# Kernel tuning notes

Hardware: AMD Instinct MI355X
Metric: run time of the kernel (lower is better)

The kernel has to match this reference:

```python
import jax, jax.numpy as jnp
import numpy as np

B, L, H = 2, 2048, 1536
I, N, R, K = 3072, 16, 96, 4


def setup_inputs() -> dict:
    key = jax.random.key(0)
    ks = jax.random.split(key, 10)
    rn = lambda k, shape, s: jax.random.normal(k, shape, jnp.float32) * s
    return {
        "hidden_states": rn(ks[0], (B, L, H), 1.0),
        "W_in": rn(ks[1], (2 * I, H), 0.02),
        "conv_w": rn(ks[2], (I, K), 0.1),
        "conv_b": rn(ks[3], (I,), 0.1),
        "W_x": rn(ks[4], (R + 2 * N, I), 0.02),
        "W_dt": rn(ks[5], (I, R), 0.02),
        "dt_bias": rn(ks[6], (I,), 0.1),
        # vLLM's weight loader stores A = -exp(A_log); replicate that here
        "A": -jnp.exp(rn(ks[7], (I, N), 0.5)),
        "D": jnp.ones((I,), jnp.float32),
        "W_out": rn(ks[8], (H, I), 0.02),
    }


def reference(hidden_states, W_in, conv_w, conv_b, W_x, W_dt, dt_bias, A, D, W_out):
    b, l, _ = hidden_states.shape
    k = conv_w.shape[1]
    n = A.shape[1]
    r = W_dt.shape[1]

    # in_proj -> [B,L,2I], split into ssm input x and gate
    proj = jnp.einsum("blh,eh->ble", hidden_states, W_in)
    x, gate = jnp.split(proj, 2, axis=-1)  # each [B,L,I]

    # causal depthwise conv1d over L (pad K-1 on the left) + SiLU
    xp = jnp.pad(x, ((0, 0), (k - 1, 0), (0, 0)))
    conv = sum(xp[:, j : j + l, :] * conv_w[:, j] for j in range(k)) + conv_b
    x = jax.nn.silu(conv)  # [B,L,I]

    # x_proj -> dt (rank R), B, C (each N)
    ssm_p = jnp.einsum("bli,pi->blp", x, W_x)
    dt_in, Bm, Cm = jnp.split(ssm_p, [r, r + n], axis=-1)

    # dt_proj (skip_bias_add) then softplus(dt + bias) inside the scan math
    dt = jnp.einsum("blr,ir->bli", dt_in, W_dt)
    delta = jax.nn.softplus(dt + dt_bias)  # [B,L,I]

    # selective scan: s_t = exp(delta_t * A) * s_{t-1} + delta_t * x_t * B_t
    def step(state, inp):
        d_t, u_t, B_t, C_t = inp  # [B,I], [B,I], [B,N], [B,N]
        dA = jnp.exp(d_t[..., None] * A)  # [B,I,N]
        state = state * dA + (d_t * u_t)[..., None] * B_t[:, None, :]
        y = jnp.einsum("bin,bn->bi", state, C_t)
        return state, y

    init = jnp.zeros((b, x.shape[-1], n), jnp.float32)
    _, ys = jax.lax.scan(
        step,
        init,
        (
            delta.transpose(1, 0, 2),
            x.transpose(1, 0, 2),
            Bm.transpose(1, 0, 2),
            Cm.transpose(1, 0, 2),
        ),
    )
    y = ys.transpose(1, 0, 2) + x * D  # skip connection via D
    y = y * jax.nn.silu(gate)

    # out_proj -> [B,L,H]
    return jnp.einsum("bli,hi->blh", y, W_out)
```

## Files before the change

kernel.cpp:

```cpp
#include <hip/hip_runtime.h>

typedef __attribute__((ext_vector_type(8))) short bf16x8;
typedef __attribute__((ext_vector_type(4))) float f32x4;

#define CCH 32
#define TCH 64

__device__ __forceinline__ unsigned short f2b(float f) {
    unsigned u = __float_as_uint(f);
    return (unsigned short)((u + 0x7fffu + ((u >> 16) & 1u)) >> 16);
}
__device__ __forceinline__ float b2f(unsigned short h) {
    return __uint_as_float(((unsigned)h) << 16);
}
__device__ __forceinline__ float softplus_f(float z) {
    return (z > 15.f) ? z : __logf(1.f + __expf(z));
}
__device__ __forceinline__ float silu_f(float g) {
    return g / (1.f + __expf(-g));
}

__device__ __forceinline__ void gload16(const unsigned short* g, unsigned short* l) {
    __builtin_amdgcn_global_load_lds(
        (const __attribute__((address_space(1))) void*)g,
        (__attribute__((address_space(3))) void*)l, 16, 0, 0);
}

__global__ __launch_bounds__(256)
void cast_all(const float* __restrict__ h, const float* __restrict__ win,
              const float* __restrict__ wx, const float* __restrict__ wdt,
              const float* __restrict__ wout,
              unsigned short* __restrict__ dh, unsigned short* __restrict__ dwin,
              unsigned short* __restrict__ dwx, unsigned short* __restrict__ dwdt,
              unsigned short* __restrict__ dwout) {
    const int n0 = 1572864, n1 = n0 + 2359296, n2 = n1 + 98304,
              n3 = n2 + 73728, n4 = n3 + 1179648;
    int i = blockIdx.x * 256 + threadIdx.x;
    const float* s; unsigned short* d; int off;
    if (i < n0)      { s = h;    d = dh;    off = i; }
    else if (i < n1) { s = win;  d = dwin;  off = i - n0; }
    else if (i < n2) { s = wx;   d = dwx;   off = i - n1; }
    else if (i < n3) { s = wdt;  d = dwdt;  off = i - n2; }
    else if (i < n4) { s = wout; d = dwout; off = i - n3; }
    else return;
    float4 v = reinterpret_cast<const float4*>(s)[off];
    ushort4 o;
    o.x = f2b(v.x); o.y = f2b(v.y); o.z = f2b(v.z); o.w = f2b(v.w);
    reinterpret_cast<ushort4*>(d)[off] = o;
}

template <int OP>
__global__ __launch_bounds__(512)
void gemm256(const unsigned short* __restrict__ A, const unsigned short* __restrict__ W,
             void* __restrict__ Cout, int Kc, int lda, int ldw, int ldc,
             int ntx, int silu_col0, long long czs) {
    __shared__ __align__(16) unsigned short lds[65536];
    const int tid  = threadIdx.x;
    const int lane = tid & 63;
    const int wave = tid >> 6;
    const int wr   = wave >> 2;
    const int wc   = wave & 3;
    const int lr   = lane & 15;
    const int quad = lane >> 4;
    const int sw   = lr & 7;

    const int nwg = gridDim.x;
    const int wg  = blockIdx.x;
    const int wgs = (wg & 7) * (nwg >> 3) + (wg >> 3);
    const int bm  = (wgs / ntx) * 256;
    const int bn  = (wgs % ntx) * 256;
    const int kz  = blockIdx.z;
    A += (size_t)kz * Kc;
    W += (size_t)kz * Kc;

    const int rsub = wave * 8 + (lane >> 3);
    const int csw  = ((lane & 7) ^ ((lane >> 3) & 7)) * 8;
    const unsigned short* gA = A + (size_t)(bm + rsub) * lda + csw;
    const unsigned short* gB = W + (size_t)(bn + rsub) * ldw + csw;

#define STA(b, h, kt) do { \
        gload16(gA + (size_t)((h) * 128) * lda + (kt) * 64,      &lds[(b) * 16384 + (h) * 8192 + wave * 512]); \
        gload16(gA + (size_t)((h) * 128 + 64) * lda + (kt) * 64, &lds[(b) * 16384 + (h) * 8192 + 4096 + wave * 512]); \
    } while (0)
#define STB(b, h, kt) do { \
        gload16(gB + (size_t)((h) * 128) * ldw + (kt) * 64,      &lds[32768 + (b) * 16384 + (h) * 8192 + wave * 512]); \
        gload16(gB + (size_t)((h) * 128 + 64) * ldw + (kt) * 64, &lds[32768 + (b) * 16384 + (h) * 8192 + 4096 + wave * 512]); \
    } while (0)

#define LDA_F(b, mh, mi, kk) \
    (*reinterpret_cast<const bf16x8*>(&lds[(b) * 16384 + ((mh) * 128 + wr * 64 + (mi) * 16 + lr) * 64 + (((((kk) << 2) | quad)) ^ sw) * 8]))
#define LDB_F(b, nh, ni, kk) \
    (*reinterpret_cast<const bf16x8*>(&lds[32768 + (b) * 16384 + ((nh) * 128 + wc * 32 + (ni) * 16 + lr) * 64 + (((((kk) << 2) | quad)) ^ sw) * 8]))

#define RD_A(b, mh) do { \
        _Pragma("unroll") for (int mi = 0; mi < 4; ++mi) { \
            fa[mi][0] = LDA_F(b, mh, mi, 0); \
            fa[mi][1] = LDA_F(b, mh, mi, 1); } } while (0)
#define RD_B(b, nh, dst) do { \
        _Pragma("unroll") for (int ni = 0; ni < 2; ++ni) { \
            dst[ni][0] = LDB_F(b, nh, ni, 0); \
            dst[ni][1] = LDB_F(b, nh, ni, 1); } } while (0)

#define MFMA_Q(mh, nh, bb) do { \
        _Pragma("unroll") for (int mi = 0; mi < 4; ++mi) \
        _Pragma("unroll") for (int ni = 0; ni < 2; ++ni) { \
            acc[(mh) * 4 + mi][(nh) * 2 + ni] = __builtin_amdgcn_mfma_f32_16x16x32_bf16(fa[mi][0], bb[ni][0], acc[(mh) * 4 + mi][(nh) * 2 + ni], 0, 0, 0); \
            acc[(mh) * 4 + mi][(nh) * 2 + ni] = __builtin_amdgcn_mfma_f32_16x16x32_bf16(fa[mi][1], bb[ni][1], acc[(mh) * 4 + mi][(nh) * 2 + ni], 0, 0, 0); } } while (0)

#define MIDB  asm volatile("s_barrier" ::: "memory")
#define LGKM0 asm volatile("s_waitcnt lgkmcnt(0)" ::: "memory")
#define ENDB  asm volatile("s_barrier" ::: "memory")
#define ENDB_VM4 asm volatile("s_waitcnt vmcnt(4)\n\ts_barrier" ::: "memory")
#define ENDB_VM0 asm volatile("s_waitcnt vmcnt(0)\n\ts_barrier" ::: "memory")
#define PRIO1 __builtin_amdgcn_s_setprio(1)
#define PRIO0 __builtin_amdgcn_s_setprio(0)

    f32x4 acc[8][4];
    const f32x4 zero = {0.f, 0.f, 0.f, 0.f};
#pragma unroll
    for (int m = 0; m < 8; ++m)
#pragma unroll
        for (int n = 0; n < 4; ++n) acc[m][n] = zero;

    bf16x8 fa[4][2], fb0[2][2], fb1[2][2];

    const int nkt = Kc >> 6;
    const int NT2 = nkt >> 1;

    STA(0, 0, 0); STB(0, 0, 0); STA(0, 1, 0); STB(0, 1, 0);
    STA(1, 0, 1); STB(1, 0, 1);
    ENDB_VM4;

#pragma unroll 1
    for (int t = 0; t < NT2 - 1; ++t) {
        const int k1 = 2 * t + 1, k2 = 2 * t + 2, k3 = 2 * t + 3;
        RD_A(0, 0); RD_B(0, 0, fb0); STA(1, 1, k1);
        MIDB; LGKM0; PRIO1; MFMA_Q(0, 0, fb0); PRIO0; ENDB;
        RD_B(0, 1, fb1); STB(1, 1, k1);
        MIDB; LGKM0; PRIO1; MFMA_Q(0, 1, fb1); PRIO0; ENDB;
        RD_A(0, 1); STA(0, 0, k2);
        MIDB; LGKM0; PRIO1; MFMA_Q(1, 0, fb0); PRIO0; ENDB;
        STB(0, 0, k2);
        MIDB; PRIO1; MFMA_Q(1, 1, fb1); PRIO0; ENDB_VM4;
        RD_A(1, 0); RD_B(1, 0, fb0); STA(0, 1, k2);
        MIDB; LGKM0; PRIO1; MFMA_Q(0, 0, fb0); PRIO0; ENDB;
        RD_B(1, 1, fb1); STB(0, 1, k2);
        MIDB; LGKM0; PRIO1; MFMA_Q(0, 1, fb1); PRIO0; ENDB;
        RD_A(1, 1); STA(1, 0, k3);
        MIDB; LGKM0; PRIO1; MFMA_Q(1, 0, fb0); PRIO0; ENDB;
        STB(1, 0, k3);
        MIDB; PRIO1; MFMA_Q(1, 1, fb1); PRIO0; ENDB_VM4;
    }
    {
        const int k1 = nkt - 1;
        RD_A(0, 0); RD_B(0, 0, fb0); STA(1, 1, k1);
        MIDB; LGKM0; PRIO1; MFMA_Q(0, 0, fb0); PRIO0; ENDB;
        RD_B(0, 1, fb1); STB(1, 1, k1);
        MIDB; LGKM0; PRIO1; MFMA_Q(0, 1, fb1); PRIO0; ENDB;
        RD_A(0, 1);
        MIDB; LGKM0; PRIO1; MFMA_Q(1, 0, fb0); PRIO0; ENDB;
        MIDB; PRIO1; MFMA_Q(1, 1, fb1); PRIO0; ENDB_VM0;
        RD_A(1, 0); RD_B(1, 0, fb0);
        MIDB; LGKM0; PRIO1; MFMA_Q(0, 0, fb0); PRIO0; ENDB;
        RD_B(1, 1, fb1);
        MIDB; LGKM0; PRIO1; MFMA_Q(0, 1, fb1); PRIO0; ENDB;
        RD_A(1, 1);
        MIDB; LGKM0; PRIO1; MFMA_Q(1, 0, fb0); PRIO0; ENDB;
        MIDB; PRIO1; MFMA_Q(1, 1, fb1); PRIO0;
    }

#pragma unroll
    for (int m = 0; m < 8; ++m) {
        const int row0 = bm + (m >> 2) * 128 + wr * 64 + (m & 3) * 16 + quad * 4;
#pragma unroll
        for (int n = 0; n < 4; ++n) {
            const int col = bn + (n >> 1) * 128 + wc * 32 + (n & 1) * 16 + lr;
#pragma unroll
            for (int reg = 0; reg < 4; ++reg) {
                float v = acc[m][n][reg];
                if (OP == 0) {
                    float* Cf = (float*)Cout + (size_t)kz * czs;
                    Cf[(size_t)(row0 + reg) * ldc + col] = v;
                } else {
                    if (col >= silu_col0) v = silu_f(v);
                    ((unsigned short*)Cout)[(size_t)(row0 + reg) * ldc + col] = f2b(v);
                }
            }
        }
    }
#undef STA
#undef STB
#undef LDA_F
#undef LDB_F
#undef RD_A
#undef RD_B
#undef MFMA_Q
#undef MIDB
#undef LGKM0
#undef ENDB
#undef ENDB_VM4
#undef ENDB_VM0
#undef PRIO1
#undef PRIO0
}

template <int OP>
__global__ __launch_bounds__(256)
void gemm_mfma(const unsigned short* __restrict__ A, const unsigned short* __restrict__ W,
               void* __restrict__ Cout, int Kc, int lda, int ldw, int ldc,
               const float* __restrict__ bias, int silu_col0, long long czs) {
    __shared__ unsigned short As[3][4096];
    __shared__ unsigned short Bs[3][4096];
    const int tid = threadIdx.x;
    const int bm = blockIdx.y * 128;
    const int bn = blockIdx.x * 128;
    const int kz = blockIdx.z;
    A += (size_t)kz * Kc;
    W += (size_t)kz * Kc;
    const int lane = tid & 63;
    const int wave = tid >> 6;
    const int r_a = lane >> 2;
    const int k8 = (lane & 3) * 8;

    const unsigned short* gA0 = A + (size_t)(bm + wave * 16 + r_a) * lda + k8;
    const unsigned short* gA1 = A + (size_t)(bm + 64 + wave * 16 + r_a) * lda + k8;
    const unsigned short* gB0 = W + (size_t)(bn + wave * 16 + r_a) * ldw + k8;
    const unsigned short* gB1 = W + (size_t)(bn + 64 + wave * 16 + r_a) * ldw + k8;

    const int wm = (wave & 1) * 64;
    const int wn = (wave >> 1) * 64;
    const int lr = lane & 15;
    const int quad = lane >> 4;

    f32x4 acc[4][4];
    const f32x4 zero = {0.f, 0.f, 0.f, 0.f};
#pragma unroll
    for (int i = 0; i < 4; i++)
#pragma unroll
        for (int j = 0; j < 4; j++) acc[i][j] = zero;

#define STAGE(koff, j) do { \
        gload16(gA0 + (koff), As[j] + wave * 512); \
        gload16(gA1 + (koff), As[j] + (wave + 4) * 512); \
        gload16(gB0 + (koff), Bs[j] + wave * 512); \
        gload16(gB1 + (koff), Bs[j] + (wave + 4) * 512); \
    } while (0)

    const int niter = Kc >> 5;
    STAGE(0, 0);
    if (niter > 1) STAGE(32, 1);

    int ib = 0;
    for (int k = 0; k < niter; k++) {
        if (k + 1 < niter)
            asm volatile("s_waitcnt vmcnt(4)\n\ts_barrier" ::: "memory");
        else
            asm volatile("s_waitcnt vmcnt(0)\n\ts_barrier" ::: "memory");
        if (k + 2 < niter) {
            int is_ = ib + 2; if (is_ >= 3) is_ -= 3;
            STAGE((k + 2) << 5, is_);
        }
        const unsigned short* as = As[ib];
        const unsigned short* bs = Bs[ib];
        bf16x8 fa[4], fb[4];
#pragma unroll
        for (int mi = 0; mi < 4; mi++)
            fa[mi] = *reinterpret_cast<const bf16x8*>(as + (wm + mi * 16 + lr) * 32 + quad * 8);
#pragma unroll
        for (int ni = 0; ni < 4; ni++)
            fb[ni] = *reinterpret_cast<const bf16x8*>(bs + (wn + ni * 16 + lr) * 32 + quad * 8);
#pragma unroll
        for (int mi = 0; mi < 4; mi++)
#pragma unroll
            for (int ni = 0; ni < 4; ni++)
                acc[mi][ni] = __builtin_amdgcn_mfma_f32_16x16x32_bf16(fa[mi], fb[ni], acc[mi][ni], 0, 0, 0);
        ib = (ib == 2) ? 0 : ib + 1;
    }
#undef STAGE

#pragma unroll
    for (int mi = 0; mi < 4; mi++)
#pragma unroll
        for (int reg = 0; reg < 4; reg++) {
            int row = bm + wm + mi * 16 + quad * 4 + reg;
#pragma unroll
            for (int ni = 0; ni < 4; ni++) {
                int col = bn + wn + ni * 16 + lr;
                float v = acc[mi][ni][reg];
                if (OP == 0) {
                    float* Cf = (float*)Cout + (size_t)kz * czs;
                    Cf[(size_t)row * ldc + col] = v;
                } else if (OP == 2) {
                    if (col >= silu_col0) v = silu_f(v);
                    ((unsigned short*)Cout)[(size_t)row * ldc + col] = f2b(v);
                } else {
                    ((unsigned short*)Cout)[(size_t)row * ldc + col] = f2b(softplus_f(v + bias[col]));
                }
            }
        }
}

__global__ __launch_bounds__(256)
void reduce_out(const float* __restrict__ p, float* __restrict__ out, int n4) {
    int i = blockIdx.x * 256 + threadIdx.x;
    if (i >= n4) return;
    float4 a = reinterpret_cast<const float4*>(p)[i];
    float4 b = reinterpret_cast<const float4*>(p + (size_t)n4 * 4)[i];
    float4 o = {a.x + b.x, a.y + b.y, a.z + b.z, a.w + b.w};
    reinterpret_cast<float4*>(out)[i] = o;
}

__global__ __launch_bounds__(256)
void reduce_xpart(const float* __restrict__ xpart, float* __restrict__ ssmp,
                  unsigned short* __restrict__ dtin) {
    const int BL = 4096;
    int idx = blockIdx.x * 256 + threadIdx.x;
    int row = idx >> 5;
    int c4 = (idx & 31) * 4;
    float4 s = {0.f, 0.f, 0.f, 0.f};
#pragma unroll
    for (int z = 0; z < 8; z++) {
        float4 v = *reinterpret_cast<const float4*>(xpart + (size_t)z * BL * 128 + (size_t)row * 128 + c4);
        s.x += v.x; s.y += v.y; s.z += v.z; s.w += v.w;
    }
    *reinterpret_cast<float4*>(ssmp + (size_t)row * 128 + c4) = s;
    if (c4 < 96) {
        ushort4 o;
        o.x = f2b(s.x); o.y = f2b(s.y); o.z = f2b(s.z); o.w = f2b(s.w);
        *reinterpret_cast<ushort4*>(dtin + (size_t)row * 96 + c4) = o;
    }
}

__global__ __launch_bounds__(256)
void conv_silu8(const unsigned short* __restrict__ projbf, const float* __restrict__ cw,
                const float* __restrict__ cb, unsigned short* __restrict__ xc) {
    const int I = 3072, L = 2048, LD = 6144;
    int idx = blockIdx.x * 256 + threadIdx.x;
    int i8 = (idx % (I / 8)) * 8;
    int bl = idx / (I / 8);
    int l = bl & (L - 1);
    float s[8];
    {
        float4 b0 = *reinterpret_cast<const float4*>(cb + i8);
        float4 b1 = *reinterpret_cast<const float4*>(cb + i8 + 4);
        s[0]=b0.x; s[1]=b0.y; s[2]=b0.z; s[3]=b0.w; s[4]=b1.x; s[5]=b1.y; s[6]=b1.z; s[7]=b1.w;
    }
    float w[8][4];
#pragma unroll
    for (int c = 0; c < 8; c++) {
        float4 wr = *reinterpret_cast<const float4*>(cw + (i8 + c) * 4);
        w[c][0]=wr.x; w[c][1]=wr.y; w[c][2]=wr.z; w[c][3]=wr.w;
    }
#pragma unroll
    for (int j = 0; j < 4; j++) {
        if (l + j - 3 >= 0) {
            uint4 r = *reinterpret_cast<const uint4*>(projbf + (size_t)(bl + j - 3) * LD + i8);
            float xv[8];
            xv[0]=b2f((unsigned short)(r.x & 0xffff)); xv[1]=b2f((unsigned short)(r.x >> 16));
            xv[2]=b2f((unsigned short)(r.y & 0xffff)); xv[3]=b2f((unsigned short)(r.y >> 16));
            xv[4]=b2f((unsigned short)(r.z & 0xffff)); xv[5]=b2f((unsigned short)(r.z >> 16));
            xv[6]=b2f((unsigned short)(r.w & 0xffff)); xv[7]=b2f((unsigned short)(r.w >> 16));
#pragma unroll
            for (int c = 0; c < 8; c++) s[c] = fmaf(xv[c], w[c][j], s[c]);
        }
    }
    unsigned short o[8];
#pragma unroll
    for (int c = 0; c < 8; c++) o[c] = f2b(silu_f(s[c]));
    uint4 packed;
    packed.x = (unsigned)o[0] | ((unsigned)o[1] << 16);
    packed.y = (unsigned)o[2] | ((unsigned)o[3] << 16);
    packed.z = (unsigned)o[4] | ((unsigned)o[5] << 16);
    packed.w = (unsigned)o[6] | ((unsigned)o[7] << 16);
    *reinterpret_cast<uint4*>(xc + (size_t)bl * I + i8) = packed;
}

__global__ __launch_bounds__(256)
void scan_passA(const unsigned short* __restrict__ delta_bf, const unsigned short* __restrict__ xc,
                const float* __restrict__ ssmp, const float* __restrict__ Aw,
                float* __restrict__ S_local, float* __restrict__ sumDelta) {
    const int I = 3072, L = 2048;
    __shared__ float bc[TCH][32];
    int g = blockIdx.x * 256 + threadIdx.x;
    int i = g % I;
    int bcid = g / I;
    int c = bcid % CCH;
    int b = bcid / CCH;
    size_t rowbase = (size_t)b * L + (size_t)c * TCH;
    for (int e = threadIdx.x; e < TCH * 8; e += 256) {
        int t = e >> 3, q = e & 7;
        float4 v = *reinterpret_cast<const float4*>(ssmp + (rowbase + t) * 128 + 96 + q * 4);
        *reinterpret_cast<float4*>(&bc[t][q * 4]) = v;
    }
    __syncthreads();

    float Arow[16];
#pragma unroll
    for (int n = 0; n < 16; n++) Arow[n] = Aw[i * 16 + n];
    float st[16];
#pragma unroll
    for (int n = 0; n < 16; n++) st[n] = 0.f;
    float sumD = 0.f;

    size_t rowI = rowbase * I + i;
    for (int t = 0; t < TCH; t++) {
        float delta = b2f(delta_bf[rowI]);
        float du = delta * b2f(xc[rowI]);
        sumD += delta;
        float4 b0 = *reinterpret_cast<const float4*>(&bc[t][0]);
        float4 b1 = *reinterpret_cast<const float4*>(&bc[t][4]);
        float4 b2 = *reinterpret_cast<const float4*>(&bc[t][8]);
        float4 b3 = *reinterpret_cast<const float4*>(&bc[t][12]);
        const float bv[16] = {b0.x,b0.y,b0.z,b0.w, b1.x,b1.y,b1.z,b1.w,
                              b2.x,b2.y,b2.z,b2.w, b3.x,b3.y,b3.z,b3.w};
#pragma unroll
        for (int n = 0; n < 16; n++)
            st[n] = fmaf(st[n], __expf(delta * Arow[n]), du * bv[n]);
        rowI += I;
    }
    size_t obase = (size_t)bcid * 16 * I + i;
#pragma unroll
    for (int n = 0; n < 16; n++) S_local[obase + (size_t)n * I] = st[n];
    sumDelta[(size_t)bcid * I + i] = sumD;
}

__global__ __launch_bounds__(256)
void scan_passB(const float* __restrict__ S_local, const float* __restrict__ sumDelta,
                const float* __restrict__ Aw, float* __restrict__ state_in) {
    const int I = 3072;
    int g = blockIdx.x * 256 + threadIdx.x;
    int i = g % I;
    int bn = g / I;
    int n = bn & 15;
    int b = bn >> 4;
    float a = Aw[i * 16 + n];
    float state = 0.f;
    for (int c = 0; c < CCH; c++) {
        int bcid = b * CCH + c;
        size_t idx = ((size_t)bcid * 16 + n) * I + i;
        state_in[idx] = state;
        state = fmaf(state, __expf(a * sumDelta[(size_t)bcid * I + i]), S_local[idx]);
    }
}

__global__ __launch_bounds__(256)
void scan_passC(const unsigned short* __restrict__ projbf,
                const unsigned short* __restrict__ xc,
                const float* __restrict__ ssmp, const unsigned short* __restrict__ delta_bf,
                const float* __restrict__ Aw, const float* __restrict__ Dw,
                const float* __restrict__ state_in, unsigned short* __restrict__ ybf) {
    const int I = 3072, L = 2048, LD = 6144;
    __shared__ float bc[TCH][32];
    int g = blockIdx.x * 256 + threadIdx.x;
    int i = g % I;
    int bcid = g / I;
    int c = bcid % CCH;
    int b = bcid / CCH;
    size_t rowbase = (size_t)b * L + (size_t)c * TCH;
    for (int e = threadIdx.x; e < TCH * 8; e += 256) {
        int t = e >> 3, q = e & 7;
        float4 v = *reinterpret_cast<const float4*>(ssmp + (rowbase + t) * 128 + 96 + q * 4);
        *reinterpret_cast<float4*>(&bc[t][q * 4]) = v;
    }
    __syncthreads();

    float Arow[16];
#pragma unroll
    for (int n = 0; n < 16; n++) Arow[n] = Aw[i * 16 + n];
    float Dv = Dw[i];
    float st[16];
    size_t sbase = (size_t)bcid * 16 * I + i;
#pragma unroll
    for (int n = 0; n < 16; n++) st[n] = state_in[sbase + (size_t)n * I];

    size_t rowI = rowbase * I + i;
    size_t rowG = rowbase * LD + I + i;
    for (int t = 0; t < TCH; t++) {
        float delta = b2f(delta_bf[rowI]);
        float u = b2f(xc[rowI]);
        float du = delta * u;
        float4 b0 = *reinterpret_cast<const float4*>(&bc[t][0]);
        float4 b1 = *reinterpret_cast<const float4*>(&bc[t][4]);
        float4 b2 = *reinterpret_cast<const float4*>(&bc[t][8]);
        float4 b3 = *reinterpret_cast<const float4*>(&bc[t][12]);
        float4 c0 = *reinterpret_cast<const float4*>(&bc[t][16]);
        float4 c1 = *reinterpret_cast<const float4*>(&bc[t][20]);
        float4 c2 = *reinterpret_cast<const float4*>(&bc[t][24]);
        float4 c3 = *reinterpret_cast<const float4*>(&bc[t][28]);
        const float bv[16] = {b0.x,b0.y,b0.z,b0.w, b1.x,b1.y,b1.z,b1.w,
                              b2.x,b2.y,b2.z,b2.w, b3.x,b3.y,b3.z,b3.w};
        const float cv[16] = {c0.x,c0.y,c0.z,c0.w, c1.x,c1.y,c1.z,c1.w,
                              c2.x,c2.y,c2.z,c2.w, c3.x,c3.y,c3.z,c3.w};
        float y = 0.f;
#pragma unroll
        for (int n = 0; n < 16; n++) {
            st[n] = fmaf(st[n], __expf(delta * Arow[n]), du * bv[n]);
            y = fmaf(st[n], cv[n], y);
        }
        y = fmaf(u, Dv, y);
        y *= b2f(projbf[rowG]);
        ybf[rowI] = f2b(y);
        rowI += I;
        rowG += LD;
    }
}

extern "C" void kernel_launch(void* const* d_in, const int* in_sizes, int n_in,
                              void* d_out, int out_size, void* d_ws, size_t ws_size,
                              hipStream_t stream) {
    const float* hidden  = (const float*)d_in[0];
    const float* W_in    = (const float*)d_in[1];
    const float* conv_w  = (const float*)d_in[2];
    const float* conv_b  = (const float*)d_in[3];
    const float* W_x     = (const float*)d_in[4];
    const float* W_dt    = (const float*)d_in[5];
    const float* dt_bias = (const float*)d_in[6];
    const float* Aw      = (const float*)d_in[7];
    const float* Dw      = (const float*)d_in[8];
    const float* W_out   = (const float*)d_in[9];
    float* out = (float*)d_out;

    constexpr int Bsz = 2, L = 2048, H = 1536, I = 3072, R = 96;
    constexpr int BL = Bsz * L;
    constexpr int TwoI = 2 * I;

    char* base = (char*)d_ws;
    unsigned short* proj_bf  = (unsigned short*)base; base += (size_t)BL * TwoI * 2;
    unsigned short* delta_bf = (unsigned short*)base; base += (size_t)BL * I * 2;
    unsigned short* xc_bf    = (unsigned short*)base; base += (size_t)BL * I * 2;
    unsigned short* y_bf     = (unsigned short*)base; base += (size_t)BL * I * 2;
    float* ssmp              = (float*)base;          base += (size_t)BL * 128 * 4;
    float* xpart             = (float*)base;          base += (size_t)8 * BL * 128 * 4;
    unsigned short* dtin_bf  = (unsigned short*)base; base += (size_t)BL * R * 2;
    unsigned short* wx_bf    = (unsigned short*)base; base += (size_t)128 * I * 2;
    unsigned short* wdt_bf   = (unsigned short*)base; base += (size_t)I * R * 2;
    unsigned short* wout_bf  = (unsigned short*)base; base += (size_t)H * I * 2;
    unsigned short* h_bf     = (unsigned short*)base; base += (size_t)BL * H * 2;
    unsigned short* win_bf   = (unsigned short*)base; base += (size_t)TwoI * H * 2;
    float* S_local  = (float*)h_bf;
    float* sumDelta = S_local + (size_t)Bsz * CCH * 16 * I;
    float* state_in = sumDelta + (size_t)Bsz * CCH * I;
    float* opart = (float*)proj_bf;

    dim3 blk(256);

    cast_all<<<(5283840 + 255) / 256, blk, 0, stream>>>(
        hidden, W_in, W_x, W_dt, W_out, h_bf, win_bf, wx_bf, wdt_bf, wout_bf);

    gemm256<2><<<dim3(24 * 16, 1, 1), dim3(512), 0, stream>>>(
        h_bf, win_bf, proj_bf, H, H, H, TwoI,  TwoI / 256,  I, 0);

    conv_silu8<<<BL * I / 8 / 256, blk, 0, stream>>>(proj_bf, conv_w, conv_b, xc_bf);

    gemm_mfma<0><<<dim3(1, BL / 128, 8), blk, 0, stream>>>(
        xc_bf, wx_bf, xpart, I / 8, I, I, 128, nullptr, 0, (long long)BL * 128);
    reduce_xpart<<<BL * 32 / 256, blk, 0, stream>>>(xpart, ssmp, dtin_bf);

    gemm_mfma<3><<<dim3(I / 128, BL / 128, 1), blk, 0, stream>>>(
        dtin_bf, wdt_bf, delta_bf, R, R, R, I, dt_bias, 0, 0);

    scan_passA<<<Bsz * I * CCH / 256, blk, 0, stream>>>(
        delta_bf, xc_bf, ssmp, Aw, S_local, sumDelta);
    scan_passB<<<Bsz * 16 * I / 256, blk, 0, stream>>>(
        S_local, sumDelta, Aw, state_in);
    scan_passC<<<Bsz * I * CCH / 256, blk, 0, stream>>>(
        proj_bf, xc_bf, ssmp, delta_bf, Aw, Dw, state_in, y_bf);

    gemm256<0><<<dim3(6 * 16, 1, 2), dim3(512), 0, stream>>>(
        y_bf, wout_bf, opart, I / 2, I, I, H,  H / 256, 0, (long long)BL * H);
    reduce_out<<<BL * H / 4 / 256, blk, 0, stream>>>(opart, out, BL * H / 4);
}
```

Measured before the change: 471.3 us.

## Prefetch full next K-tile in gemm256 and remap workgroups for XCD locality

The gemm256 prologue now loads both halves of the second K-tile, and the main loop issues the next tile's loads earlier in each phase, waiting with vmcnt(8) instead of vmcnt(4). This deepens the global-to-LDS prefetch so MFMA phases are less likely to stall on memory. Workgroup-to-tile mapping also changes: each of the 8 XCDs (blockIdx & 7) gets a contiguous band of columns, or of rows when the column count is not a multiple of 8, to improve L2 reuse of shared operand panels. The cost is more loads in flight per wave and a tighter LDS buffer reuse schedule, which depends on barrier ordering staying correct.

New measurement: 473.5 us. About the same (+0.5%).

```diff
diff --git a/kernel.cpp b/kernel.cpp
--- a/kernel.cpp
+++ b/kernel.cpp
@@ -53,7 +53,7 @@
 __global__ __launch_bounds__(512)
 void gemm256(const unsigned short* __restrict__ A, const unsigned short* __restrict__ W,
              void* __restrict__ Cout, int Kc, int lda, int ldw, int ldc,
-             int ntx, int silu_col0, long long czs) {
+             int ntx, int nty, int silu_col0, long long czs) {
     __shared__ __align__(16) unsigned short lds[65536];
     const int tid  = threadIdx.x;
     const int lane = tid & 63;
@@ -64,12 +64,21 @@
     const int quad = lane >> 4;
     const int sw   = lr & 7;
 
-    const int nwg = gridDim.x;
-    const int wg  = blockIdx.x;
-    const int wgs = (wg & 7) * (nwg >> 3) + (wg >> 3);
-    const int bm  = (wgs / ntx) * 256;
-    const int bn  = (wgs % ntx) * 256;
-    const int kz  = blockIdx.z;
+    const int c = blockIdx.x & 7;
+    const int j = blockIdx.x >> 3;
+    int bm_t, bn_t;
+    if ((ntx & 7) == 0) {
+        const int cpx = ntx >> 3;
+        bn_t = c * cpx + j % cpx;
+        bm_t = j / cpx;
+    } else {
+        const int rpx = nty >> 3;
+        bm_t = c * rpx + j % rpx;
+        bn_t = j / rpx;
+    }
+    const int bm = bm_t * 256;
+    const int bn = bn_t * 256;
+    const int kz = blockIdx.z;
     A += (size_t)kz * Kc;
     W += (size_t)kz * Kc;
 
@@ -110,7 +119,7 @@
 #define MIDB  asm volatile("s_barrier" ::: "memory")
 #define LGKM0 asm volatile("s_waitcnt lgkmcnt(0)" ::: "memory")
 #define ENDB  asm volatile("s_barrier" ::: "memory")
-#define ENDB_VM4 asm volatile("s_waitcnt vmcnt(4)\n\ts_barrier" ::: "memory")
+#define ENDB_VM8 asm volatile("s_waitcnt vmcnt(8)\n\ts_barrier" ::: "memory")
 #define ENDB_VM0 asm volatile("s_waitcnt vmcnt(0)\n\ts_barrier" ::: "memory")
 #define PRIO1 __builtin_amdgcn_s_setprio(1)
 #define PRIO0 __builtin_amdgcn_s_setprio(0)
@@ -128,34 +137,33 @@
     const int NT2 = nkt >> 1;
 
     STA(0, 0, 0); STB(0, 0, 0); STA(0, 1, 0); STB(0, 1, 0);
-    STA(1, 0, 1); STB(1, 0, 1);
-    ENDB_VM4;
+    STA(1, 0, 1); STB(1, 0, 1); STA(1, 1, 1); STB(1, 1, 1);
+    ENDB_VM8;
 
 #pragma unroll 1
     for (int t = 0; t < NT2 - 1; ++t) {
-        const int k1 = 2 * t + 1, k2 = 2 * t + 2, k3 = 2 * t + 3;
-        RD_A(0, 0); RD_B(0, 0, fb0); STA(1, 1, k1);
+        const int k2 = 2 * t + 2, k3 = 2 * t + 3;
+        RD_A(0, 0); RD_B(0, 0, fb0);
         MIDB; LGKM0; PRIO1; MFMA_Q(0, 0, fb0); PRIO0; ENDB;
-        RD_B(0, 1, fb1); STB(1, 1, k1);
+        RD_B(0, 1, fb1); STA(0, 0, k2); STB(0, 0, k2);
         MIDB; LGKM0; PRIO1; MFMA_Q(0, 1, fb1); PRIO0; ENDB;
-        RD_A(0, 1); STA(0, 0, k2);
+        RD_A(0, 1); STB(0, 1, k2);
         MIDB; LGKM0; PRIO1; MFMA_Q(1, 0, fb0); PRIO0; ENDB;
-        STB(0, 0, k2);
-        MIDB; PRIO1; MFMA_Q(1, 1, fb1); PRIO0; ENDB_VM4;
-        RD_A(1, 0); RD_B(1, 0, fb0); STA(0, 1, k2);
+        STA(0, 1, k2);
+        MIDB; PRIO1; MFMA_Q(1, 1, fb1); PRIO0; ENDB_VM8;
+        RD_A(1, 0); RD_B(1, 0, fb0);
         MIDB; LGKM0; PRIO1; MFMA_Q(0, 0, fb0); PRIO0; ENDB;
-        RD_B(1, 1, fb1); STB(0, 1, k2);
+        RD_B(1, 1, fb1); STA(1, 0, k3); STB(1, 0, k3);
         MIDB; LGKM0; PRIO1; MFMA_Q(0, 1, fb1); PRIO0; ENDB;
-        RD_A(1, 1); STA(1, 0, k3);
+        RD_A(1, 1); STB(1, 1, k3);
         MIDB; LGKM0; PRIO1; MFMA_Q(1, 0, fb0); PRIO0; ENDB;
-        STB(1, 0, k3);
-        MIDB; PRIO1; MFMA_Q(1, 1, fb1); PRIO0; ENDB_VM4;
+        STA(1, 1, k3);
+        MIDB; PRIO1; MFMA_Q(1, 1, fb1); PRIO0; ENDB_VM8;
     }
     {
-        const int k1 = nkt - 1;
-        RD_A(0, 0); RD_B(0, 0, fb0); STA(1, 1, k1);
+        RD_A(0, 0); RD_B(0, 0, fb0);
         MIDB; LGKM0; PRIO1; MFMA_Q(0, 0, fb0); PRIO0; ENDB;
-        RD_B(0, 1, fb1); STB(1, 1, k1);
+        RD_B(0, 1, fb1);
         MIDB; LGKM0; PRIO1; MFMA_Q(0, 1, fb1); PRIO0; ENDB;
         RD_A(0, 1);
         MIDB; LGKM0; PRIO1; MFMA_Q(1, 0, fb0); PRIO0; ENDB;
@@ -198,7 +206,7 @@
 #undef MIDB
 #undef LGKM0
 #undef ENDB
-#undef ENDB_VM4
+#undef ENDB_VM8
 #undef ENDB_VM0
 #undef PRIO1
 #undef PRIO0
@@ -548,7 +556,8 @@
         hidden, W_in, W_x, W_dt, W_out, h_bf, win_bf, wx_bf, wdt_bf, wout_bf);
 
     gemm256<2><<<dim3(24 * 16, 1, 1), dim3(512), 0, stream>>>(
-        h_bf, win_bf, proj_bf, H, H, H, TwoI,  TwoI / 256,  I, 0);
+        h_bf, win_bf, proj_bf, H, H, H, TwoI,  TwoI / 256,  BL / 256,
+         I, 0);
 
     conv_silu8<<<BL * I / 8 / 256, blk, 0, stream>>>(proj_bf, conv_w, conv_b, xc_bf);
 
@@ -567,6 +576,7 @@
         proj_bf, xc_bf, ssmp, delta_bf, Aw, Dw, state_in, y_bf);
 
     gemm256<0><<<dim3(6 * 16, 1, 2), dim3(512), 0, stream>>>(
-        y_bf, wout_bf, opart, I / 2, I, I, H,  H / 256, 0, (long long)BL * H);
+        y_bf, wout_bf, opart, I / 2, I, I, H,  H / 256,  BL / 256,
+        0, (long long)BL * H);
     reduce_out<<<BL * H / 4 / 256, blk, 0, stream>>>(opart, out, BL * H / 4);
 }
```

## Replace split-K out-projection GEMM and reduction with single 256x128-tile kernel

Applied to the files above, without the earlier changes.

The out-projection previously ran as a split-K=2 GEMM with 256x256 tiles over 96 blocks, writing fp32 partials that a separate kernel summed. It now runs as one kernel with 256x128 tiles over the full K across 192 blocks. Operands are double-buffered in LDS through direct global-to-LDS loads, with an XOR swizzle and an L2-friendly block ordering. This drops the partial-buffer write, the reread and one launch. In exchange each block has a longer K loop and synchronizes on a full vmcnt(0) barrier every step, which may expose load latency.

New measurement: 471.4 us. About the same (+0.0%).

```diff
diff --git a/kernel.cpp b/kernel.cpp
--- a/kernel.cpp
+++ b/kernel.cpp
@@ -204,6 +204,118 @@
 #undef PRIO0
 }
 
+__global__ __launch_bounds__(512)
+void gemm_out(const unsigned short* __restrict__ A, const unsigned short* __restrict__ W,
+              float* __restrict__ Cout, int Kc, int lda, int ldw, int ldc) {
+    __shared__ __align__(16) unsigned short A0s[16384];
+    __shared__ __align__(16) unsigned short B0s[8192];
+    __shared__ __align__(16) unsigned short A1s[16384];
+    __shared__ __align__(16) unsigned short B1s[8192];
+    const int tid  = threadIdx.x;
+    const int lane = tid & 63;
+    const int wave = tid >> 6;
+    const int wr   = wave >> 2;
+    const int wc   = wave & 3;
+    const int lr   = lane & 15;
+    const int quad = lane >> 4;
+    const int sw   = lr & 7;
+
+    const int c = blockIdx.x & 7;
+    const int j = blockIdx.x >> 3;
+    const int bm = (c * 2 + (j & 1)) * 256;
+    const int bn = (j >> 1) * 128;
+
+    const int rsub = wave * 8 + (lane >> 3);
+    const int csw  = ((lane & 7) ^ ((lane >> 3) & 7)) * 8;
+    const unsigned short* gA = A + (size_t)(bm + rsub) * lda + csw;
+    const unsigned short* gB = W + (size_t)(bn + rsub) * ldw + csw;
+
+#define STAGE_A(ARR, kt) do { \
+        gload16(gA + (size_t)0   * lda + (kt) * 64, ARR + 0     + wave * 512); \
+        gload16(gA + (size_t)64  * lda + (kt) * 64, ARR + 4096  + wave * 512); \
+        gload16(gA + (size_t)128 * lda + (kt) * 64, ARR + 8192  + wave * 512); \
+        gload16(gA + (size_t)192 * lda + (kt) * 64, ARR + 12288 + wave * 512); \
+    } while (0)
+#define STAGE_B(ARR, kt) do { \
+        gload16(gB + (size_t)0   * ldw + (kt) * 64, ARR + 0     + wave * 512); \
+        gload16(gB + (size_t)64  * ldw + (kt) * 64, ARR + 4096  + wave * 512); \
+    } while (0)
+
+#define LDA_F(ARR, m, kk) \
+    (*reinterpret_cast<const bf16x8*>(&ARR[(wr * 128 + (m) * 16 + lr) * 64 + (((((kk) << 2) | quad)) ^ sw) * 8]))
+#define LDB_F(ARR, ni, kk) \
+    (*reinterpret_cast<const bf16x8*>(&ARR[(wc * 32 + (ni) * 16 + lr) * 64 + (((((kk) << 2) | quad)) ^ sw) * 8]))
+
+#define PRIO1 __builtin_amdgcn_s_setprio(1)
+#define PRIO0 __builtin_amdgcn_s_setprio(0)
+#define VM0B  asm volatile("s_waitcnt vmcnt(0)\n\ts_barrier" ::: "memory")
+
+#define TILE_BODY(AX, BX) do { \
+        _Pragma("unroll") for (int ni = 0; ni < 2; ++ni) { \
+            fb[ni][0] = LDB_F(BX, ni, 0); fb[ni][1] = LDB_F(BX, ni, 1); } \
+        _Pragma("unroll") for (int m = 0; m < 4; ++m) { \
+            fa0[m][0] = LDA_F(AX, m, 0); fa0[m][1] = LDA_F(AX, m, 1); } \
+        PRIO1; \
+        _Pragma("unroll") for (int m = 0; m < 4; ++m) \
+        _Pragma("unroll") for (int ni = 0; ni < 2; ++ni) { \
+            acc[m][ni] = __builtin_amdgcn_mfma_f32_16x16x32_bf16(fa0[m][0], fb[ni][0], acc[m][ni], 0, 0, 0); \
+            acc[m][ni] = __builtin_amdgcn_mfma_f32_16x16x32_bf16(fa0[m][1], fb[ni][1], acc[m][ni], 0, 0, 0); } \
+        PRIO0; \
+        _Pragma("unroll") for (int m = 0; m < 4; ++m) { \
+            fa1[m][0] = LDA_F(AX, m + 4, 0); fa1[m][1] = LDA_F(AX, m + 4, 1); } \
+        PRIO1; \
+        _Pragma("unroll") for (int m = 0; m < 4; ++m) \
+        _Pragma("unroll") for (int ni = 0; ni < 2; ++ni) { \
+            acc[m + 4][ni] = __builtin_amdgcn_mfma_f32_16x16x32_bf16(fa1[m][0], fb[ni][0], acc[m + 4][ni], 0, 0, 0); \
+            acc[m + 4][ni] = __builtin_amdgcn_mfma_f32_16x16x32_bf16(fa1[m][1], fb[ni][1], acc[m + 4][ni], 0, 0, 0); } \
+        PRIO0; \
+    } while (0)
+
+    f32x4 acc[8][2];
+    const f32x4 zero = {0.f, 0.f, 0.f, 0.f};
+#pragma unroll
+    for (int m = 0; m < 8; ++m) { acc[m][0] = zero; acc[m][1] = zero; }
+
+    bf16x8 fa0[4][2], fa1[4][2], fb[2][2];
+
+    const int nkt = Kc >> 6;
+
+    STAGE_A(A0s, 0); STAGE_B(B0s, 0);
+    VM0B;
+
+#pragma unroll 1
+    for (int t = 0; t < nkt; t += 2) {
+        if (t + 1 < nkt) { STAGE_A(A1s, t + 1); STAGE_B(B1s, t + 1); }
+        TILE_BODY(A0s, B0s);
+        VM0B;
+        if (t + 1 < nkt) {
+            if (t + 2 < nkt) { STAGE_A(A0s, t + 2); STAGE_B(B0s, t + 2); }
+            TILE_BODY(A1s, B1s);
+            VM0B;
+        }
+    }
+
+#pragma unroll
+    for (int m = 0; m < 8; ++m) {
+        const int row0 = bm + wr * 128 + m * 16 + quad * 4;
+#pragma unroll
+        for (int ni = 0; ni < 2; ++ni) {
+            const int col = bn + wc * 32 + ni * 16 + lr;
+#pragma unroll
+            for (int reg = 0; reg < 4; ++reg)
+                Cout[(size_t)(row0 + reg) * ldc + col] = acc[m][ni][reg];
+        }
+    }
+#undef STAGE_A
+#undef STAGE_B
+#undef LDA_F
+#undef LDB_F
+#undef PRIO1
+#undef PRIO0
+#undef VM0B
+#undef TILE_BODY
+}
+
 template <int OP>
 __global__ __launch_bounds__(256)
 void gemm_mfma(const unsigned short* __restrict__ A, const unsigned short* __restrict__ W,
@@ -298,16 +410,6 @@
                 }
             }
         }
-}
-
-__global__ __launch_bounds__(256)
-void reduce_out(const float* __restrict__ p, float* __restrict__ out, int n4) {
-    int i = blockIdx.x * 256 + threadIdx.x;
-    if (i >= n4) return;
-    float4 a = reinterpret_cast<const float4*>(p)[i];
-    float4 b = reinterpret_cast<const float4*>(p + (size_t)n4 * 4)[i];
-    float4 o = {a.x + b.x, a.y + b.y, a.z + b.z, a.w + b.w};
-    reinterpret_cast<float4*>(out)[i] = o;
 }
 
 __global__ __launch_bounds__(256)
@@ -540,7 +642,6 @@
     float* S_local  = (float*)h_bf;
     float* sumDelta = S_local + (size_t)Bsz * CCH * 16 * I;
     float* state_in = sumDelta + (size_t)Bsz * CCH * I;
-    float* opart = (float*)proj_bf;
 
     dim3 blk(256);
 
@@ -566,7 +667,6 @@
     scan_passC<<<Bsz * I * CCH / 256, blk, 0, stream>>>(
         proj_bf, xc_bf, ssmp, delta_bf, Aw, Dw, state_in, y_bf);
 
-    gemm256<0><<<dim3(6 * 16, 1, 2), dim3(512), 0, stream>>>(
-        y_bf, wout_bf, opart, I / 2, I, I, H,  H / 256, 0, (long long)BL * H);
-    reduce_out<<<BL * H / 4 / 256, blk, 0, stream>>>(opart, out, BL * H / 4);
-}
+    gemm_out<<<dim3(192, 1, 1), dim3(512), 0, stream>>>(
+        y_bf, wout_bf, out, I, I, I, H);
+}
```
